# Optimization experiments

Hardware: AMD Instinct MI355X
Metric: run time of the kernel (lower is better)

Reference implementation:

```python
import jax, jax.numpy as jnp
from jax import lax
import numpy as np
import math

ORDER = 5            # bessel_order
CUTOFF = 25e9        # cutoff_hz
FS = 100e9           # sampling rate
B, T = 64, 131072    # batch, time samples


def _bessel_ba(order, cutoff, fs):
    """numpy re-implementation of scipy.signal.bessel(order, cutoff, fs=fs, norm='mag')."""
    n = order
    # reverse Bessel polynomial theta_n(s), highest power first (monic)
    c = np.array([math.factorial(2 * n - k) / (2.0 ** (n - k) * math.factorial(k) * math.factorial(n - k))
                  for k in range(n, -1, -1)])
    p = np.roots(c)            # analog prototype poles
    a0 = c[-1]                 # DC gain numerator (H(s) = a0 / theta(s))
    # 'mag' norm: find w3 with |H(jw3)| = 1/sqrt(2)  <=>  |theta(jw3)|^2 = 2*a0^2
    f = lambda w: np.abs(np.polyval(c, 1j * w)) ** 2 - 2.0 * a0 ** 2
    lo, hi = 0.0, 1.0
    while f(hi) < 0.0:
        hi *= 2.0
    for _ in range(200):
        mid = 0.5 * (lo + hi)
        if f(mid) < 0.0:
            lo = mid
        else:
            hi = mid
    w3 = 0.5 * (lo + hi)
    p = p / w3
    k = a0 / w3 ** n
    # prewarp + lowpass-to-lowpass
    warped = 2.0 * fs * np.tan(np.pi * cutoff / fs)
    p = p * warped
    k = k * warped ** n
    # bilinear transform (zeros of analog prototype: none -> n zeros at z=-1)
    fs2 = 2.0 * fs
    pz = (fs2 + p) / (fs2 - p)
    kz = k / np.real(np.prod(fs2 - p))
    b = kz * np.real(np.poly(-np.ones(n)))
    a = np.real(np.poly(pz))
    return b, a


def setup_inputs() -> dict:
    key = jax.random.key(0)
    x = jax.random.normal(key, (B, T), dtype=jnp.float32)
    b, a = _bessel_ba(ORDER, CUTOFF, FS)
    return {"x": x,
            "b": jnp.asarray(b, jnp.float32),
            "a": jnp.asarray(a, jnp.float32)}


def _lfilter(x, a, b):
    """Direct-form I IIR filter along last axis; x: (B, T), a/b: (N+1,)."""
    a0 = a[0]
    bn = b / a0
    an = a / a0
    nb = bn.shape[0]
    # FIR part f[t] = sum_j b[j] * x[t-j] via causal convolution
    f = lax.conv_general_dilated(
        x[:, None, :], jnp.flip(bn)[None, None, :],
        window_strides=(1,), padding=[(nb - 1, 0)],
        dimension_numbers=("NCH", "OIH", "NCH"))[:, 0, :]          # (B, T)
    ar = an[1:]                   # (N,) feedback taps a[1..N]
    N = ar.shape[0]
    def step(carry, f_t):         # carry: (B, N) = [y[t-1], ..., y[t-N]]
        y_t = f_t - carry @ ar    # (B,)
        carry = jnp.concatenate([y_t[:, None], carry[:, :-1]], axis=1)
        return carry, y_t
    _, y = lax.scan(step, jnp.zeros((x.shape[0], N), x.dtype), f.T)
    return y.T                    # (B, T)


def reference(x, b, a):
    xmax = jnp.max(jnp.abs(x))
    return xmax * _lfilter(x / xmax, a, b)
```

## Files before the change

### kernel.cpp

```cpp
#include <hip/hip_runtime.h>


constexpr int T_LEN   = 131072;
constexpr int B_ROWS  = 64;
constexpr int CHUNK   = 64;
constexpr int WARM    = 64;
constexpr int CPR     = T_LEN / CHUNK;

__global__ __launch_bounds__(256) void bessel_iir_kernel(
    const float* __restrict__ x,
    const float* __restrict__ bco,
    const float* __restrict__ aco,
    float* __restrict__ y)
{
    const int tid = blockIdx.x * blockDim.x + threadIdx.x;
    const int row = tid / CPR;
    const int c   = tid % CPR;

    const float* __restrict__ xr = x + (size_t)row * T_LEN;
    float* __restrict__       yr = y + (size_t)row * T_LEN;

    const float inv = 1.0f / aco[0];
    const float b0 = bco[0] * inv, b1 = bco[1] * inv, b2 = bco[2] * inv,
                b3 = bco[3] * inv, b4 = bco[4] * inv, b5 = bco[5] * inv;
    const float a1 = aco[1] * inv, a2 = aco[2] * inv, a3 = aco[3] * inv,
                a4 = aco[4] * inv, a5 = aco[5] * inv;

    const int t0 = c * CHUNK;
    const int ts = t0 - WARM;

    float y1 = 0.f, y2 = 0.f, y3 = 0.f, y4 = 0.f, y5 = 0.f;
    float xm1 = 0.f, xm2 = 0.f, xm3 = 0.f, xm4 = 0.f, xm5 = 0.f;

    auto step4 = [&](const float4 xv, float4& out) {
        float f0 = b0*xv.x + b1*xm1 + b2*xm2 + b3*xm3 + b4*xm4 + b5*xm5;
        float o0 = f0 - a1*y1 - a2*y2 - a3*y3 - a4*y4 - a5*y5;
        float f1 = b0*xv.y + b1*xv.x + b2*xm1 + b3*xm2 + b4*xm3 + b5*xm4;
        float o1 = f1 - a1*o0 - a2*y1 - a3*y2 - a4*y3 - a5*y4;
        float f2 = b0*xv.z + b1*xv.y + b2*xv.x + b3*xm1 + b4*xm2 + b5*xm3;
        float o2 = f2 - a1*o1 - a2*o0 - a3*y1 - a4*y2 - a5*y3;
        float f3 = b0*xv.w + b1*xv.z + b2*xv.y + b3*xv.x + b4*xm1 + b5*xm2;
        float o3 = f3 - a1*o2 - a2*o1 - a3*o0 - a4*y1 - a5*y2;
        y5 = y1;  y4 = o0; y3 = o1; y2 = o2; y1 = o3;
        xm5 = xm1; xm4 = xv.x; xm3 = xv.y; xm2 = xv.z; xm1 = xv.w;
        out.x = o0; out.y = o1; out.z = o2; out.w = o3;
    };

    if (c > 0) {
        if (ts >= 5) {
            xm1 = xr[ts-1]; xm2 = xr[ts-2]; xm3 = xr[ts-3];
            xm4 = xr[ts-4]; xm5 = xr[ts-5];
        }
        #pragma unroll 4
        for (int t = ts; t < t0; t += 4) {
            float4 xv = *(const float4*)(xr + t);
            float4 dump;
            step4(xv, dump);
        }
    }

    #pragma unroll 4
    for (int t = t0; t < t0 + CHUNK; t += 4) {
        float4 xv = *(const float4*)(xr + t);
        float4 ov;
        step4(xv, ov);
        *(float4*)(yr + t) = ov;
    }
}

extern "C" void kernel_launch(void* const* d_in, const int* in_sizes, int n_in,
                              void* d_out, int out_size, void* d_ws, size_t ws_size,
                              hipStream_t stream) {
    const float* x   = (const float*)d_in[0];
    const float* bco = (const float*)d_in[1];
    const float* aco = (const float*)d_in[2];
    float* y = (float*)d_out;

    const int total_threads = B_ROWS * CPR;
    const int block = 256;
    const int grid  = total_threads / block;
    bessel_iir_kernel<<<grid, block, 0, stream>>>(x, bco, aco, y);
}
```

Baseline: 100.8 us.

## Stage input and output tiles through padded LDS for coalesced IIR chunks

Each block now loads a contiguous span of the row plus a warm-up halo into padded shared memory with coalesced float4 reads. Threads run the IIR recurrence on their chunk out of LDS and write results back to LDS, and the block then stores them with coalesced float4 writes. Chunk size drops from 64 to 32 while the warm-up stays at 64, so there are more parallel chains but the redundant warm-up work grows relative to useful output. The old per-thread strided global reads are removed, and the change adds barriers and LDS traffic in exchange.

```diff
diff --git a/kernel.cpp b/kernel.cpp
--- a/kernel.cpp
+++ b/kernel.cpp
@@ -1,24 +1,57 @@
 #include <hip/hip_runtime.h>
 
 
-constexpr int T_LEN   = 131072;
-constexpr int B_ROWS  = 64;
-constexpr int CHUNK   = 64;
-constexpr int WARM    = 64;
-constexpr int CPR     = T_LEN / CHUNK;
+constexpr int T_LEN  = 131072;
+constexpr int B_ROWS = 64;
+constexpr int CHUNK  = 32;
+constexpr int WARM   = 64;
+constexpr int HEAD   = 96;
+constexpr int BLOCK  = 256;
+constexpr int SPAN   = BLOCK * CHUNK;
+constexpr int BPR    = T_LEN / SPAN;
+constexpr int XTOT   = HEAD + SPAN;
+constexpr int XPAD   = XTOT + XTOT / 32;
+constexpr int YPAD   = SPAN + SPAN / 32;
 
-__global__ __launch_bounds__(256) void bessel_iir_kernel(
+__device__ __forceinline__ int padi(int s) { return s + (s >> 5); }
+
+__global__ __launch_bounds__(BLOCK, 2) void bessel_tile_kernel(
     const float* __restrict__ x,
     const float* __restrict__ bco,
     const float* __restrict__ aco,
     float* __restrict__ y)
 {
-    const int tid = blockIdx.x * blockDim.x + threadIdx.x;
-    const int row = tid / CPR;
-    const int c   = tid % CPR;
+    __shared__ float xs[XPAD];
+    __shared__ float ys[YPAD];
+
+    const int b    = blockIdx.x;
+    const int row  = b / BPR;
+    const int tile = b % BPR;
+    const int base = tile * SPAN;
+    const int j    = threadIdx.x;
 
     const float* __restrict__ xr = x + (size_t)row * T_LEN;
     float* __restrict__       yr = y + (size_t)row * T_LEN;
+
+    if (tile == 0) {
+        for (int s = j; s < HEAD; s += BLOCK)
+            xs[padi(s)] = 0.0f;
+        #pragma unroll
+        for (int it = 0; it < SPAN / 4 / BLOCK; ++it) {
+            int k = j + it * BLOCK;
+            float4 v = *(const float4*)(xr + base + 4 * k);
+            int S = HEAD + 4 * k;
+            int p = padi(S);
+            xs[p] = v.x; xs[p + 1] = v.y; xs[p + 2] = v.z; xs[p + 3] = v.w;
+        }
+    } else {
+        for (int k = j; k < XTOT / 4; k += BLOCK) {
+            float4 v = *(const float4*)(xr + base - HEAD + 4 * k);
+            int S = 4 * k;
+            int p = padi(S);
+            xs[p] = v.x; xs[p + 1] = v.y; xs[p + 2] = v.z; xs[p + 3] = v.w;
+        }
+    }
 
     const float inv = 1.0f / aco[0];
     const float b0 = bco[0] * inv, b1 = bco[1] * inv, b2 = bco[2] * inv,
@@ -26,45 +59,43 @@
     const float a1 = aco[1] * inv, a2 = aco[2] * inv, a3 = aco[3] * inv,
                 a4 = aco[4] * inv, a5 = aco[5] * inv;
 
-    const int t0 = c * CHUNK;
-    const int ts = t0 - WARM;
+    __syncthreads();
 
-    float y1 = 0.f, y2 = 0.f, y3 = 0.f, y4 = 0.f, y5 = 0.f;
-    float xm1 = 0.f, xm2 = 0.f, xm3 = 0.f, xm4 = 0.f, xm5 = 0.f;
+    {
+        const int S0 = HEAD + j * CHUNK;
+        const int ws = S0 - WARM;
+        float y1 = 0.f, y2 = 0.f, y3 = 0.f, y4 = 0.f, y5 = 0.f;
+        float xm1 = xs[padi(ws - 1)], xm2 = xs[padi(ws - 2)], xm3 = xs[padi(ws - 3)],
+              xm4 = xs[padi(ws - 4)], xm5 = xs[padi(ws - 5)];
 
-    auto step4 = [&](const float4 xv, float4& out) {
-        float f0 = b0*xv.x + b1*xm1 + b2*xm2 + b3*xm3 + b4*xm4 + b5*xm5;
-        float o0 = f0 - a1*y1 - a2*y2 - a3*y3 - a4*y4 - a5*y5;
-        float f1 = b0*xv.y + b1*xv.x + b2*xm1 + b3*xm2 + b4*xm3 + b5*xm4;
-        float o1 = f1 - a1*o0 - a2*y1 - a3*y2 - a4*y3 - a5*y4;
-        float f2 = b0*xv.z + b1*xv.y + b2*xv.x + b3*xm1 + b4*xm2 + b5*xm3;
-        float o2 = f2 - a1*o1 - a2*o0 - a3*y1 - a4*y2 - a5*y3;
-        float f3 = b0*xv.w + b1*xv.z + b2*xv.y + b3*xv.x + b4*xm1 + b5*xm2;
-        float o3 = f3 - a1*o2 - a2*o1 - a3*o0 - a4*y1 - a5*y2;
-        y5 = y1;  y4 = o0; y3 = o1; y2 = o2; y1 = o3;
-        xm5 = xm1; xm4 = xv.x; xm3 = xv.y; xm2 = xv.z; xm1 = xv.w;
-        out.x = o0; out.y = o1; out.z = o2; out.w = o3;
-    };
-
-    if (c > 0) {
-        if (ts >= 5) {
-            xm1 = xr[ts-1]; xm2 = xr[ts-2]; xm3 = xr[ts-3];
-            xm4 = xr[ts-4]; xm5 = xr[ts-5];
+        #pragma unroll 8
+        for (int t = ws; t < S0; ++t) {
+            float xv = xs[padi(t)];
+            float f = b0 * xv + b1 * xm1 + b2 * xm2 + b3 * xm3 + b4 * xm4 + b5 * xm5;
+            float o = f - a1 * y1 - a2 * y2 - a3 * y3 - a4 * y4 - a5 * y5;
+            y5 = y4; y4 = y3; y3 = y2; y2 = y1; y1 = o;
+            xm5 = xm4; xm4 = xm3; xm3 = xm2; xm2 = xm1; xm1 = xv;
         }
-        #pragma unroll 4
-        for (int t = ts; t < t0; t += 4) {
-            float4 xv = *(const float4*)(xr + t);
-            float4 dump;
-            step4(xv, dump);
+        #pragma unroll 8
+        for (int t = S0; t < S0 + CHUNK; ++t) {
+            float xv = xs[padi(t)];
+            float f = b0 * xv + b1 * xm1 + b2 * xm2 + b3 * xm3 + b4 * xm4 + b5 * xm5;
+            float o = f - a1 * y1 - a2 * y2 - a3 * y3 - a4 * y4 - a5 * y5;
+            y5 = y4; y4 = y3; y3 = y2; y2 = y1; y1 = o;
+            xm5 = xm4; xm4 = xm3; xm3 = xm2; xm2 = xm1; xm1 = xv;
+            ys[padi(t - HEAD)] = o;
         }
     }
 
-    #pragma unroll 4
-    for (int t = t0; t < t0 + CHUNK; t += 4) {
-        float4 xv = *(const float4*)(xr + t);
-        float4 ov;
-        step4(xv, ov);
-        *(float4*)(yr + t) = ov;
+    __syncthreads();
+
+    #pragma unroll
+    for (int it = 0; it < SPAN / 4 / BLOCK; ++it) {
+        int S = 4 * (j + it * BLOCK);
+        int p = padi(S);
+        float4 v;
+        v.x = ys[p]; v.y = ys[p + 1]; v.z = ys[p + 2]; v.w = ys[p + 3];
+        *(float4*)(yr + base + S) = v;
     }
 }
 
@@ -76,8 +107,6 @@
     const float* aco = (const float*)d_in[2];
     float* y = (float*)d_out;
 
-    const int total_threads = B_ROWS * CPR;
-    const int block = 256;
-    const int grid  = total_threads / block;
-    bessel_iir_kernel<<<grid, block, 0, stream>>>(x, bco, aco, y);
+    const int grid = B_ROWS * BPR;
+    bessel_tile_kernel<<<grid, BLOCK, 0, stream>>>(x, bco, aco, y);
 }
```

Result: faster. 97.92 us (-2.8%).
